# Kernel tuning notes

Measured on AMD Instinct MI355X. Metric: run time of the kernel, lower is better.

The kernel has to match this reference:

```python
import jax, jax.numpy as jnp
import numpy as np

B, L, H = 8, 2048, 1024

def setup_inputs() -> dict:
    key = jax.random.key(0)
    k1, k2, k3, k4 = jax.random.split(key, 4)
    inputs = jax.random.normal(k1, (B, L, H), dtype=jnp.float32)
    mask = jax.random.normal(k2, (B, L, L), dtype=jnp.float32) * 0.01
    W = jax.random.normal(k3, (H, H), dtype=jnp.float32) * (1.0 / np.sqrt(H))
    b = jax.random.normal(k4, (H,), dtype=jnp.float32) * 0.01
    return {"inputs": inputs, "mask": mask, "W": W, "b": b}

def reference(inputs, mask, W, b):
    # q = Linear(inputs): [B, L, H]
    q = jnp.einsum('blh,oh->blo', inputs, W) + b
    # u = q @ inputs^T: [B, L, L]  (no 1/sqrt(d) scaling)
    u = jnp.einsum('blh,bmh->blm', q, inputs)
    u = jax.nn.relu(u)  # relu=True
    a = jax.nn.softmax(u, axis=2)
    a = a + mask  # mask added AFTER softmax
    h = jnp.einsum('blm,bmh->blh', a, inputs)
    return (h, a)
```

## Files before the change

### kernel.cpp

```cpp
#include <hip/hip_runtime.h>

#define Bb 8
#define Ll 2048
#define Hh 1024

typedef __bf16 bf16;
typedef signed char i8;
typedef __attribute__((ext_vector_type(8))) __bf16 bf16x8;
typedef __attribute__((ext_vector_type(4))) __bf16 bf16x4;
typedef __attribute__((ext_vector_type(4))) float f32x4;
typedef __attribute__((ext_vector_type(4))) int i32x4;

#define RQ 6.0f
#define SQ (RQ / 16320.f)

__device__ __forceinline__ void gload16(const void* src, void* dst) {
  __builtin_amdgcn_global_load_lds(
      (const __attribute__((address_space(1))) void*)src,
      (__attribute__((address_space(3))) void*)dst, 16, 0, 0);
}

__device__ __forceinline__ void q16(float v, float inv_s, i8* h, i8* l) {
  float vs = fminf(fmaxf(v * inv_s, -16319.f), 16319.f);
  float hf = rintf(vs * 0.0078125f);
  *h = (i8)(int)hf;
  *l = (i8)__float2int_rn(vs - 128.f * hf);
}

__global__ __launch_bounds__(256) void split_x_k(
    const float* __restrict__ X, bf16* __restrict__ Xhi,
    bf16* __restrict__ Xlo, i8* __restrict__ Xhi8, i8* __restrict__ Xlo8,
    bf16* __restrict__ XT) {
  __shared__ float tile[64][65];
  const int h0 = blockIdx.x << 6, l0 = blockIdx.y << 6, b = blockIdx.z;
  const int t = threadIdx.x;
  const int c = t & 63, r0 = t >> 6;
  const long base = ((long)b * Ll + l0) * Hh + h0;
  const float* Xb = X + base;
  const float inv_s = 1.f / SQ;
#pragma unroll
  for (int i = 0; i < 16; ++i) {
    int row = (i << 2) + r0;
    long o = base + (long)row * Hh + c;
    float x = Xb[(long)row * Hh + c];
    bf16 hi = (bf16)x;
    Xhi[o] = hi;
    Xlo[o] = (bf16)(x - (float)hi);
    i8 qh, ql;
    q16(x, inv_s, &qh, &ql);
    Xhi8[o] = qh;
    Xlo8[o] = ql;
    tile[row][c] = x;
  }
  __syncthreads();
  bf16* XTB = XT + ((long)b * Hh + h0) * Ll + l0;
#pragma unroll
  for (int i = 0; i < 16; ++i) {
    int row = (i << 2) + r0;
    XTB[(long)row * Ll + c] = (bf16)tile[c][row];
  }
}

__global__ __launch_bounds__(256) void split_w_k(
    const float* __restrict__ W, bf16* __restrict__ Whi,
    bf16* __restrict__ Wlo) {
  int i = blockIdx.x * 256 + threadIdx.x;
  float4 v = ((const float4*)W)[i];
  float vv[4] = {v.x, v.y, v.z, v.w};
#pragma unroll
  for (int j = 0; j < 4; ++j) {
    float x = vv[j];
    bf16 hi = (bf16)x;
    Whi[i * 4 + j] = hi;
    Wlo[i * 4 + j] = (bf16)(x - (float)hi);
  }
}

__global__ __launch_bounds__(256, 2) void gemm1_k(
    const bf16* __restrict__ Ahi, const bf16* __restrict__ Alo,
    const bf16* __restrict__ Bhi, const bf16* __restrict__ Blo,
    i8* __restrict__ outQhi8, i8* __restrict__ outQlo8,
    const float* __restrict__ bias) {
  constexpr int K = Hh;
  constexpr int BUFB = 32768;
  __shared__ char lds[2 * BUFB];
  const int m0 = blockIdx.y * 128, n0 = blockIdx.x * 128;
  const int t = threadIdx.x, lane = t & 63, w = t >> 6;
  const int wr = (w >> 1) * 64, wc = (w & 1) * 64;
  const int g = lane >> 4, fr = lane & 15;

  f32x4 acc[4][4];
#pragma unroll
  for (int m = 0; m < 4; ++m)
#pragma unroll
    for (int n = 0; n < 4; ++n) acc[m][n] = {0.f, 0.f, 0.f, 0.f};

  const bf16* srcs[8];
#pragma unroll
  for (int p = 0; p < 8; ++p) {
    int c = p * 256 + t;
    int mat = c >> 10, cc = c & 1023;
    int row = cc >> 3;
    int l = (cc & 7) ^ (row & 7);
    const bf16* pl = mat ? (l < 4 ? Bhi : Blo) : (l < 4 ? Ahi : Alo);
    srcs[p] = pl + (long)((mat ? n0 : m0) + row) * K + (l & 3) * 8;
  }

  auto STAGE = [&](int buf, int kt) {
    char* base = lds + buf * BUFB;
#pragma unroll
    for (int p = 0; p < 8; ++p) gload16(srcs[p] + kt, base + (p * 256 + t) * 16);
  };

  STAGE(0, 0);
  __syncthreads();
  int cur = 0;
  for (int kt = 0; kt < K; kt += 32) {
    if (kt + 32 < K) STAGE(cur ^ 1, kt + 32);
    char* base = lds + cur * BUFB;
    bf16x8 ah[4], al[4], bh[4], bl[4];
#pragma unroll
    for (int m = 0; m < 4; ++m) {
      int row = wr + m * 16 + fr;
      ah[m] = *(const bf16x8*)(base + row * 128 + ((g ^ (row & 7)) << 4));
      al[m] = *(const bf16x8*)(base + row * 128 + (((4 | g) ^ (row & 7)) << 4));
    }
#pragma unroll
    for (int n = 0; n < 4; ++n) {
      int row = wc + n * 16 + fr;
      bh[n] = *(const bf16x8*)(base + 16384 + row * 128 + ((g ^ (row & 7)) << 4));
      bl[n] = *(const bf16x8*)(base + 16384 + row * 128 + (((4 | g) ^ (row & 7)) << 4));
    }
#pragma unroll
    for (int m = 0; m < 4; ++m)
#pragma unroll
      for (int n = 0; n < 4; ++n) {
        acc[m][n] = __builtin_amdgcn_mfma_f32_16x16x32_bf16(ah[m], bh[n], acc[m][n], 0, 0, 0);
        acc[m][n] = __builtin_amdgcn_mfma_f32_16x16x32_bf16(ah[m], bl[n], acc[m][n], 0, 0, 0);
        acc[m][n] = __builtin_amdgcn_mfma_f32_16x16x32_bf16(al[m], bh[n], acc[m][n], 0, 0, 0);
      }
    __syncthreads();
    cur ^= 1;
  }

  const int crow0 = m0 + wr + (lane >> 4) * 4;
  const int ccol0 = n0 + wc + fr;
  const float inv_s = 1.f / SQ;
#pragma unroll
  for (int m = 0; m < 4; ++m)
#pragma unroll
    for (int n = 0; n < 4; ++n)
#pragma unroll
      for (int j = 0; j < 4; ++j) {
        const int r = crow0 + m * 16 + j;
        const int cc = ccol0 + n * 16;
        float v = acc[m][n][j] + bias[cc];
        i8 qh, ql;
        q16(v, inv_s, &qh, &ql);
        const long off = (long)r * Hh + cc;
        outQhi8[off] = qh;
        outQlo8[off] = ql;
      }
}

__global__ __launch_bounds__(256, 2) void gemm2_k(
    const i8* __restrict__ Ahi8, const i8* __restrict__ Alo8,
    const i8* __restrict__ Bhi8, const i8* __restrict__ Blo8,
    float* __restrict__ outF) {
  constexpr int K = Hh;
  constexpr int BUFB = 32768;
  __shared__ char lds[2 * BUFB];
  const int b = blockIdx.z;
  const int m0 = blockIdx.y * 128, n0 = blockIdx.x * 128;
  const long sAB = (long)Ll * Hh;
  const int t = threadIdx.x, lane = t & 63, w = t >> 6;
  const int wr = (w >> 1) * 64, wc = (w & 1) * 64;
  const int g = lane >> 4, fr = lane & 15;

  i32x4 HH[4][4], CX[4][4];
#pragma unroll
  for (int m = 0; m < 4; ++m)
#pragma unroll
    for (int n = 0; n < 4; ++n) {
      HH[m][n] = {0, 0, 0, 0};
      CX[m][n] = {0, 0, 0, 0};
    }

  const i8* srcs[8];
#pragma unroll
  for (int p = 0; p < 8; ++p) {
    int c = p * 256 + t;
    int mat = c >> 10, cc = c & 1023;
    int row = cc >> 3;
    int l = (cc & 7) ^ (row & 7);
    const i8* pl = mat ? (l < 4 ? Bhi8 : Blo8) : (l < 4 ? Ahi8 : Alo8);
    srcs[p] = pl + (long)b * sAB + (long)((mat ? n0 : m0) + row) * K + (l & 3) * 16;
  }

  auto STAGE = [&](int buf, int kt) {
    char* base = lds + buf * BUFB;
#pragma unroll
    for (int p = 0; p < 8; ++p) gload16(srcs[p] + kt, base + (p * 256 + t) * 16);
  };

  STAGE(0, 0);
  __syncthreads();
  int cur = 0;
  for (int kt = 0; kt < K; kt += 64) {
    if (kt + 64 < K) STAGE(cur ^ 1, kt + 64);
    char* base = lds + cur * BUFB;
    i32x4 ah8[4], al8[4], bh8[4], bl8[4];
#pragma unroll
    for (int m = 0; m < 4; ++m) {
      int row = wr + m * 16 + fr;
      ah8[m] = *(const i32x4*)(base + row * 128 + ((g ^ (row & 7)) << 4));
      al8[m] = *(const i32x4*)(base + row * 128 + (((4 | g) ^ (row & 7)) << 4));
    }
#pragma unroll
    for (int n = 0; n < 4; ++n) {
      int row = wc + n * 16 + fr;
      bh8[n] = *(const i32x4*)(base + 16384 + row * 128 + ((g ^ (row & 7)) << 4));
      bl8[n] = *(const i32x4*)(base + 16384 + row * 128 + (((4 | g) ^ (row & 7)) << 4));
    }
#pragma unroll
    for (int m = 0; m < 4; ++m)
#pragma unroll
      for (int n = 0; n < 4; ++n) {
        HH[m][n] = __builtin_amdgcn_mfma_i32_16x16x64_i8(ah8[m], bh8[n], HH[m][n], 0, 0, 0);
        CX[m][n] = __builtin_amdgcn_mfma_i32_16x16x64_i8(ah8[m], bl8[n], CX[m][n], 0, 0, 0);
        CX[m][n] = __builtin_amdgcn_mfma_i32_16x16x64_i8(al8[m], bh8[n], CX[m][n], 0, 0, 0);
      }
    __syncthreads();
    cur ^= 1;
  }

  const float C8h = (SQ * SQ) * 16384.f, C8c = (SQ * SQ) * 128.f;
  const int crow0 = m0 + wr + (lane >> 4) * 4;
  const int ccol0 = n0 + wc + fr;
#pragma unroll
  for (int m = 0; m < 4; ++m)
#pragma unroll
    for (int n = 0; n < 4; ++n)
#pragma unroll
      for (int j = 0; j < 4; ++j) {
        const int r = crow0 + m * 16 + j;
        const int cc = ccol0 + n * 16;
        float v = C8h * (float)HH[m][n][j] + C8c * (float)CX[m][n][j];
        outF[(long)b * Ll * Ll + (long)r * Ll + cc] = v > 0.f ? v : 0.f;
      }
}

__global__ __launch_bounds__(256, 2) void gemm3_k(
    const bf16* __restrict__ A, const bf16* __restrict__ Bm,
    float* __restrict__ outF) {
  constexpr int K = Ll;
  constexpr int BUFB = 32768;
  __shared__ char lds[2 * BUFB];
  const int b = blockIdx.z;
  const int m0 = blockIdx.y * 128, n0 = blockIdx.x * 128;
  const long sA = (long)Ll * Ll, sB = (long)Hh * Ll;
  const int t = threadIdx.x, lane = t & 63, w = t >> 6;
  const int wr = (w >> 1) * 64, wc = (w & 1) * 64;
  const int g = lane >> 4, fr = lane & 15;

  f32x4 acc[4][4];
#pragma unroll
  for (int m = 0; m < 4; ++m)
#pragma unroll
    for (int n = 0; n < 4; ++n) acc[m][n] = {0.f, 0.f, 0.f, 0.f};

  const bf16* srcs[8];
#pragma unroll
  for (int p = 0; p < 8; ++p) {
    int c = p * 256 + t;
    int mat = c >> 10, cc = c & 1023;
    int row = cc >> 3;
    int l = (cc & 7) ^ (row & 7);
    const bf16* pl = mat ? Bm + (long)b * sB + (long)(n0 + row) * K
                         : A + (long)b * sA + (long)(m0 + row) * K;
    srcs[p] = pl + l * 8;
  }

  auto STAGE = [&](int buf, int kt) {
    char* base = lds + buf * BUFB;
#pragma unroll
    for (int p = 0; p < 8; ++p) gload16(srcs[p] + kt, base + (p * 256 + t) * 16);
  };

  STAGE(0, 0);
  __syncthreads();
  int cur = 0;
  for (int kt = 0; kt < K; kt += 64) {
    if (kt + 64 < K) STAGE(cur ^ 1, kt + 64);
    char* base = lds + cur * BUFB;
#pragma unroll
    for (int ks = 0; ks < 2; ++ks) {
      bf16x8 ah[4], bh[4];
#pragma unroll
      for (int m = 0; m < 4; ++m) {
        int row = wr + m * 16 + fr;
        ah[m] = *(const bf16x8*)(base + row * 128 + ((((ks << 2) | g) ^ (row & 7)) << 4));
      }
#pragma unroll
      for (int n = 0; n < 4; ++n) {
        int row = wc + n * 16 + fr;
        bh[n] = *(const bf16x8*)(base + 16384 + row * 128 + ((((ks << 2) | g) ^ (row & 7)) << 4));
      }
#pragma unroll
      for (int m = 0; m < 4; ++m)
#pragma unroll
        for (int n = 0; n < 4; ++n)
          acc[m][n] = __builtin_amdgcn_mfma_f32_16x16x32_bf16(ah[m], bh[n], acc[m][n], 0, 0, 0);
    }
    __syncthreads();
    cur ^= 1;
  }

  const int crow0 = m0 + wr + (lane >> 4) * 4;
  const int ccol0 = n0 + wc + fr;
#pragma unroll
  for (int m = 0; m < 4; ++m)
#pragma unroll
    for (int n = 0; n < 4; ++n)
#pragma unroll
      for (int j = 0; j < 4; ++j) {
        const int r = crow0 + m * 16 + j;
        const int cc = ccol0 + n * 16;
        outF[(long)b * Ll * Hh + (long)r * Hh + cc] = acc[m][n][j];
      }
}

__global__ __launch_bounds__(256) void softmax_mask_k(
    float* __restrict__ U, const float* __restrict__ mask,
    bf16* __restrict__ Abf) {
  __shared__ float red[8];
  const long row = blockIdx.x;
  float* u = U + row * 2048;
  const float* mk = mask + row * 2048;
  bf16* ab = Abf + row * 2048;
  const int t = threadIdx.x;
  float4 v0 = *(const float4*)(u + t * 4);
  float4 v1 = *(const float4*)(u + 1024 + t * 4);
  float m = fmaxf(fmaxf(fmaxf(v0.x, v0.y), fmaxf(v0.z, v0.w)),
                  fmaxf(fmaxf(v1.x, v1.y), fmaxf(v1.z, v1.w)));
#pragma unroll
  for (int s = 32; s; s >>= 1) m = fmaxf(m, __shfl_xor(m, s));
  if ((t & 63) == 0) red[t >> 6] = m;
  __syncthreads();
  m = fmaxf(fmaxf(red[0], red[1]), fmaxf(red[2], red[3]));
  float e0 = __expf(v0.x - m), e1 = __expf(v0.y - m), e2 = __expf(v0.z - m),
        e3 = __expf(v0.w - m);
  float e4 = __expf(v1.x - m), e5 = __expf(v1.y - m), e6 = __expf(v1.z - m),
        e7 = __expf(v1.w - m);
  float s = ((e0 + e1) + (e2 + e3)) + ((e4 + e5) + (e6 + e7));
#pragma unroll
  for (int sh = 32; sh; sh >>= 1) s += __shfl_xor(s, sh);
  if ((t & 63) == 0) red[4 + (t >> 6)] = s;
  __syncthreads();
  s = (red[4] + red[5]) + (red[6] + red[7]);
  const float inv = 1.0f / s;
  float4 k0 = *(const float4*)(mk + t * 4);
  float4 k1 = *(const float4*)(mk + 1024 + t * 4);
  float4 a0 = {e0 * inv + k0.x, e1 * inv + k0.y, e2 * inv + k0.z,
               e3 * inv + k0.w};
  float4 a1 = {e4 * inv + k1.x, e5 * inv + k1.y, e6 * inv + k1.z,
               e7 * inv + k1.w};
  *(float4*)(u + t * 4) = a0;
  *(float4*)(u + 1024 + t * 4) = a1;
  bf16x4 b0 = {(bf16)a0.x, (bf16)a0.y, (bf16)a0.z, (bf16)a0.w};
  bf16x4 b1 = {(bf16)a1.x, (bf16)a1.y, (bf16)a1.z, (bf16)a1.w};
  *(bf16x4*)(ab + t * 4) = b0;
  *(bf16x4*)(ab + 1024 + t * 4) = b1;
}

extern "C" void kernel_launch(void* const* d_in, const int* in_sizes, int n_in,
                              void* d_out, int out_size, void* d_ws,
                              size_t ws_size, hipStream_t stream) {
  const float* X = (const float*)d_in[0];
  const float* mask = (const float*)d_in[1];
  const float* W = (const float*)d_in[2];
  const float* bias = (const float*)d_in[3];
  float* out_h = (float*)d_out;
  float* out_a = out_h + (size_t)Bb * Ll * Hh;

  const size_t NX = (size_t)Bb * Ll * Hh;
  const size_t NA = (size_t)Bb * Ll * Ll;
  const size_t NW = (size_t)Hh * Hh;
  bf16* Xhi = (bf16*)d_ws;
  bf16* Xlo = Xhi + NX;
  bf16* XT = Xlo + NX;
  bf16* Abf = XT + NX;
  bf16* Whi = Abf + NA;
  bf16* Wlo = Whi + NW;
  i8* Xhi8 = (i8*)(Wlo + NW);
  i8* Xlo8 = Xhi8 + NX;
  i8* Qhi8 = Xlo8 + NX;
  i8* Qlo8 = Qhi8 + NX;

  split_x_k<<<dim3(Hh / 64, Ll / 64, Bb), 256, 0, stream>>>(X, Xhi, Xlo,
                                                            Xhi8, Xlo8, XT);
  split_w_k<<<dim3((Hh * Hh / 4) / 256), 256, 0, stream>>>(W, Whi, Wlo);
  gemm1_k<<<dim3(Hh / 128, (Bb * Ll) / 128, 1), 256, 0, stream>>>(
      Xhi, Xlo, Whi, Wlo, Qhi8, Qlo8, bias);
  gemm2_k<<<dim3(Ll / 128, Ll / 128, Bb), 256, 0, stream>>>(
      Qhi8, Qlo8, Xhi8, Xlo8, out_a);
  softmax_mask_k<<<dim3(Bb * Ll), 256, 0, stream>>>(out_a, mask, Abf);
  gemm3_k<<<dim3(Hh / 128, Ll / 128, Bb), 256, 0, stream>>>(Abf, XT, out_h);
}
```

Before: 448.0 us.

## Use partial vmcnt waits in GEMM pipelines and swizzle block order across XCDs

```diff
diff --git a/kernel.cpp b/kernel.cpp
--- a/kernel.cpp
+++ b/kernel.cpp
@@ -26,6 +26,14 @@
   *h = (i8)(int)hf;
   *l = (i8)__float2int_rn(vs - 128.f * hf);
 }
+
+#define WAIT8_BAR()                                   \
+  asm volatile("s_waitcnt vmcnt(8)" ::: "memory");    \
+  __builtin_amdgcn_s_barrier()
+#define WAIT0_BAR()                                   \
+  asm volatile("s_waitcnt vmcnt(0)" ::: "memory");    \
+  __builtin_amdgcn_s_barrier()
+#define BAR() __builtin_amdgcn_s_barrier()
 
 __global__ __launch_bounds__(256) void split_x_k(
     const float* __restrict__ X, bf16* __restrict__ Xhi,
@@ -84,7 +92,9 @@
   constexpr int K = Hh;
   constexpr int BUFB = 32768;
   __shared__ char lds[2 * BUFB];
-  const int m0 = blockIdx.y * 128, n0 = blockIdx.x * 128;
+  const int flat = blockIdx.y * 8 + blockIdx.x;
+  const int wsw = (flat & 7) * 128 + (flat >> 3);
+  const int m0 = (wsw >> 3) * 128, n0 = (wsw & 7) * 128;
   const int t = threadIdx.x, lane = t & 63, w = t >> 6;
   const int wr = (w >> 1) * 64, wc = (w & 1) * 64;
   const int g = lane >> 4, fr = lane & 15;
@@ -112,12 +122,8 @@
     for (int p = 0; p < 8; ++p) gload16(srcs[p] + kt, base + (p * 256 + t) * 16);
   };
 
-  STAGE(0, 0);
-  __syncthreads();
-  int cur = 0;
-  for (int kt = 0; kt < K; kt += 32) {
-    if (kt + 32 < K) STAGE(cur ^ 1, kt + 32);
-    char* base = lds + cur * BUFB;
+  auto COMPUTE = [&](int buf) {
+    char* base = lds + buf * BUFB;
     bf16x8 ah[4], al[4], bh[4], bl[4];
 #pragma unroll
     for (int m = 0; m < 4; ++m) {
@@ -139,9 +145,19 @@
         acc[m][n] = __builtin_amdgcn_mfma_f32_16x16x32_bf16(ah[m], bl[n], acc[m][n], 0, 0, 0);
         acc[m][n] = __builtin_amdgcn_mfma_f32_16x16x32_bf16(al[m], bh[n], acc[m][n], 0, 0, 0);
       }
-    __syncthreads();
+  };
+
+  STAGE(0, 0);
+  int cur = 0;
+  for (int kt = 0; kt < K - 32; kt += 32) {
+    STAGE(cur ^ 1, kt + 32);
+    WAIT8_BAR();
+    COMPUTE(cur);
+    BAR();
     cur ^= 1;
   }
+  WAIT0_BAR();
+  COMPUTE(cur);
 
   const int crow0 = m0 + wr + (lane >> 4) * 4;
   const int ccol0 = n0 + wc + fr;
@@ -170,8 +186,10 @@
   constexpr int K = Hh;
   constexpr int BUFB = 32768;
   __shared__ char lds[2 * BUFB];
-  const int b = blockIdx.z;
-  const int m0 = blockIdx.y * 128, n0 = blockIdx.x * 128;
+  const int flat = (blockIdx.z * 16 + blockIdx.y) * 16 + blockIdx.x;
+  const int wsw = (flat & 7) * 256 + (flat >> 3);
+  const int b = wsw >> 8;
+  const int m0 = ((wsw >> 4) & 15) * 128, n0 = (wsw & 15) * 128;
   const long sAB = (long)Ll * Hh;
   const int t = threadIdx.x, lane = t & 63, w = t >> 6;
   const int wr = (w >> 1) * 64, wc = (w & 1) * 64;
@@ -203,12 +221,8 @@
     for (int p = 0; p < 8; ++p) gload16(srcs[p] + kt, base + (p * 256 + t) * 16);
   };
 
-  STAGE(0, 0);
-  __syncthreads();
-  int cur = 0;
-  for (int kt = 0; kt < K; kt += 64) {
-    if (kt + 64 < K) STAGE(cur ^ 1, kt + 64);
-    char* base = lds + cur * BUFB;
+  auto COMPUTE = [&](int buf) {
+    char* base = lds + buf * BUFB;
     i32x4 ah8[4], al8[4], bh8[4], bl8[4];
 #pragma unroll
     for (int m = 0; m < 4; ++m) {
@@ -230,9 +244,19 @@
         CX[m][n] = __builtin_amdgcn_mfma_i32_16x16x64_i8(ah8[m], bl8[n], CX[m][n], 0, 0, 0);
         CX[m][n] = __builtin_amdgcn_mfma_i32_16x16x64_i8(al8[m], bh8[n], CX[m][n], 0, 0, 0);
       }
-    __syncthreads();
+  };
+
+  STAGE(0, 0);
+  int cur = 0;
+  for (int kt = 0; kt < K - 64; kt += 64) {
+    STAGE(cur ^ 1, kt + 64);
+    WAIT8_BAR();
+    COMPUTE(cur);
+    BAR();
     cur ^= 1;
   }
+  WAIT0_BAR();
+  COMPUTE(cur);
 
   const float C8h = (SQ * SQ) * 16384.f, C8c = (SQ * SQ) * 128.f;
   const int crow0 = m0 + wr + (lane >> 4) * 4;
@@ -256,8 +280,10 @@
   constexpr int K = Ll;
   constexpr int BUFB = 32768;
   __shared__ char lds[2 * BUFB];
-  const int b = blockIdx.z;
-  const int m0 = blockIdx.y * 128, n0 = blockIdx.x * 128;
+  const int flat = (blockIdx.z * 16 + blockIdx.y) * 8 + blockIdx.x;
+  const int wsw = (flat & 7) * 128 + (flat >> 3);
+  const int b = wsw >> 7;
+  const int m0 = ((wsw >> 3) & 15) * 128, n0 = (wsw & 7) * 128;
   const long sA = (long)Ll * Ll, sB = (long)Hh * Ll;
   const int t = threadIdx.x, lane = t & 63, w = t >> 6;
   const int wr = (w >> 1) * 64, wc = (w & 1) * 64;
@@ -287,12 +313,8 @@
     for (int p = 0; p < 8; ++p) gload16(srcs[p] + kt, base + (p * 256 + t) * 16);
   };
 
-  STAGE(0, 0);
-  __syncthreads();
-  int cur = 0;
-  for (int kt = 0; kt < K; kt += 64) {
-    if (kt + 64 < K) STAGE(cur ^ 1, kt + 64);
-    char* base = lds + cur * BUFB;
+  auto COMPUTE = [&](int buf) {
+    char* base = lds + buf * BUFB;
 #pragma unroll
     for (int ks = 0; ks < 2; ++ks) {
       bf16x8 ah[4], bh[4];
@@ -312,9 +334,19 @@
         for (int n = 0; n < 4; ++n)
           acc[m][n] = __builtin_amdgcn_mfma_f32_16x16x32_bf16(ah[m], bh[n], acc[m][n], 0, 0, 0);
     }
-    __syncthreads();
+  };
+
+  STAGE(0, 0);
+  int cur = 0;
+  for (int kt = 0; kt < K - 64; kt += 64) {
+    STAGE(cur ^ 1, kt + 64);
+    WAIT8_BAR();
+    COMPUTE(cur);
+    BAR();
     cur ^= 1;
   }
+  WAIT0_BAR();
+  COMPUTE(cur);
 
   const int crow0 = m0 + wr + (lane >> 4) * 4;
   const int ccol0 = n0 + wc + fr;
```

New measurement: 413.5 us. 7.7% less time.
